# Kernel optimization log

Hardware: AMD Instinct MI355X
Metric: run time of the kernel (lower is better)

## Reference

```python
import jax, jax.numpy as jnp
import numpy as np

N = 1_000_000   # pose-graph nodes
E = 2_000_000   # edges (odometry + loop closures)
M = N - 1
L1, L2, L3, L4 = 1.0, 0.1, 1.0, 0.1  # loss weights
EPS = 1e-8

# ---- quaternion / Lie-group helpers (pypose convention: [x,y,z,w]) ----

def qmul(q, r):
    qv, qw = q[..., :3], q[..., 3:]
    rv, rw = r[..., :3], r[..., 3:]
    w = qw * rw - jnp.sum(qv * rv, axis=-1, keepdims=True)
    v = qw * rv + rw * qv + jnp.cross(qv, rv)
    return jnp.concatenate([v, w], axis=-1)

def qconj(q):  # inverse of a unit quaternion
    return jnp.concatenate([-q[..., :3], q[..., 3:]], axis=-1)

def qrot(q, v):  # rotate vector v by unit quaternion q
    qv, qw = q[..., :3], q[..., 3:]
    t = 2.0 * jnp.cross(qv, v)
    return v + qw * t + jnp.cross(qv, t)

def so3_log(q):  # SO3 -> so3 rotation vector phi
    v, w = q[..., :3], q[..., 3]
    n = jnp.linalg.norm(v, axis=-1)
    theta = 2.0 * jnp.arctan2(n, w)
    big = n > EPS
    k = jnp.where(big, theta / jnp.where(big, n, 1.0), 2.0 / jnp.where(jnp.abs(w) > EPS, w, 1.0))
    return v * k[..., None]

def se3_log(t, q):  # SE3 -> se3 = [tau(3), phi(3)] (translation first, pypose order)
    phi = so3_log(q)
    theta2 = jnp.sum(phi * phi, axis=-1)
    theta = jnp.sqrt(theta2)
    small = theta < 1e-4
    ts = jnp.where(small, 1.0, theta)
    # V^{-1} coefficient: 1/theta^2 - (1+cos)/(2 theta sin); Taylor -> 1/12
    coef = jnp.where(small, 1.0 / 12.0,
                     1.0 / jnp.where(small, 1.0, theta2)
                     - (1.0 + jnp.cos(ts)) / (2.0 * ts * jnp.sin(ts)))
    pxt = jnp.cross(phi, t)
    tau = t - 0.5 * pxt + coef[..., None] * jnp.cross(phi, pxt)  # V^{-1} t without 3x3 mats
    return jnp.concatenate([tau, phi], axis=-1)

def _unit_quat(key, n):
    q = jax.random.normal(key, (n, 4), dtype=jnp.float32)
    return q / jnp.linalg.norm(q, axis=-1, keepdims=True)

def setup_inputs() -> dict:
    key = jax.random.key(0)
    k = jax.random.split(key, 9)
    nodes = jnp.concatenate([jax.random.normal(k[0], (N, 3), jnp.float32), _unit_quat(k[1], N)], axis=-1)
    vels = jax.random.normal(k[2], (N, 3), jnp.float32)
    edges = jax.random.randint(k[3], (E, 2), 0, N, dtype=jnp.int32)
    poses = jnp.concatenate([jax.random.normal(k[4], (E, 3), jnp.float32), _unit_quat(k[5], E)], axis=-1)
    imu_drots = _unit_quat(k[6], M)
    imu_dtrans = 0.1 * jax.random.normal(k[7], (M, 3), jnp.float32)
    imu_dvels = 0.1 * jax.random.normal(k[8], (M, 3), jnp.float32)
    dts = jnp.full((M, 1), 0.05, dtype=jnp.float32)
    return dict(edges=edges, nodes=nodes, vels=vels, poses=poses,
                imu_drots=imu_drots, imu_dtrans=imu_dtrans, imu_dvels=imu_dvels, dts=dts)

def reference(edges, nodes, vels, poses, imu_drots, imu_dtrans, imu_dvels, dts):
    t_n, q_n = nodes[:, :3], nodes[:, 3:]
    # --- pose-graph residual: (poses^-1 o node1^-1 o node2).Log() ---
    n1 = nodes[edges[:, 0]]
    n2 = nodes[edges[:, 1]]
    t1, q1 = n1[:, :3], n1[:, 3:]
    t2, q2 = n2[:, :3], n2[:, 3:]
    tp, qp = poses[:, :3], poses[:, 3:]
    qi1 = qconj(q1)
    ti1 = -qrot(qi1, t1)           # node1^-1
    qa = qmul(qi1, q2)
    ta = ti1 + qrot(qi1, t2)       # node1^-1 o node2
    qip = qconj(qp)
    tip = -qrot(qip, tp)           # poses^-1
    qe = qmul(qip, qa)
    te = tip + qrot(qip, ta)
    pgerr = se3_log(te, qe)                                   # [E, 6]
    # --- adjacent velocity residual ---
    adjvelerr = imu_dvels - (vels[1:] - vels[:-1])            # [M, 3]
    # --- IMU rotation residual: (drot^-1 o R1^-1 o R2).Log() ---
    qre = qmul(qconj(imu_drots), qmul(qconj(q_n[:-1]), q_n[1:]))
    imuroterr = so3_log(qre)                                  # [M, 3]
    # --- translation/velocity residual ---
    transvelerr = (t_n[1:] - t_n[:-1]) - (vels[:-1] * dts + imu_dtrans)  # [M, 3]
    return jnp.concatenate([L1 * pgerr.ravel(), L2 * adjvelerr.ravel(),
                            L3 * imuroterr.ravel(), L4 * transvelerr.ravel()], axis=0)
```

## Files before the change

### kernel.cpp

```cpp
#include <hip/hip_runtime.h>
#include <math.h>

#define EPS_Q 1e-8f

struct F3 { float x, y, z; };
struct Q4 { F3 v; float w; };

typedef float fvec4 __attribute__((ext_vector_type(4)));

__device__ __forceinline__ F3 add3(F3 a, F3 b){ return {a.x+b.x, a.y+b.y, a.z+b.z}; }
__device__ __forceinline__ F3 sub3(F3 a, F3 b){ return {a.x-b.x, a.y-b.y, a.z-b.z}; }
__device__ __forceinline__ F3 scal3(float s, F3 a){ return {s*a.x, s*a.y, s*a.z}; }
__device__ __forceinline__ float dot3(F3 a, F3 b){ return a.x*b.x + a.y*b.y + a.z*b.z; }
__device__ __forceinline__ F3 cross3(F3 a, F3 b){
    return { a.y*b.z - a.z*b.y, a.z*b.x - a.x*b.z, a.x*b.y - a.y*b.x };
}

__device__ __forceinline__ Q4 qmul(Q4 q, Q4 r){
    Q4 o;
    o.w = q.w*r.w - dot3(q.v, r.v);
    o.v = add3(add3(scal3(q.w, r.v), scal3(r.w, q.v)), cross3(q.v, r.v));
    return o;
}
__device__ __forceinline__ Q4 qconj(Q4 q){ return { {-q.v.x, -q.v.y, -q.v.z}, q.w }; }
__device__ __forceinline__ F3 qrot(Q4 q, F3 v){
    F3 t = scal3(2.0f, cross3(q.v, v));
    return add3(add3(v, scal3(q.w, t)), cross3(q.v, t));
}
__device__ __forceinline__ F3 so3_log(Q4 q){
    float n = sqrtf(dot3(q.v, q.v));
    float theta = 2.0f * atan2f(n, q.w);
    float k;
    if (n > EPS_Q) k = theta / n;
    else           k = 2.0f / ((fabsf(q.w) > EPS_Q) ? q.w : 1.0f);
    return scal3(k, q.v);
}

__device__ __forceinline__ float ntl (const float* p){ return __builtin_nontemporal_load(p); }
__device__ __forceinline__ int   ntli(const int*   p){ return __builtin_nontemporal_load(p); }
__device__ __forceinline__ void  nts (float* p, float v){ __builtin_nontemporal_store(v, p); }

__global__ __launch_bounds__(256)
void fused_kernel(const int*   __restrict__ edges,
                  const float* __restrict__ nodes,
                  const float* __restrict__ vels,
                  const float* __restrict__ poses,
                  const float* __restrict__ imu_drots,
                  const float* __restrict__ imu_dtrans,
                  const float* __restrict__ imu_dvels,
                  const float* __restrict__ dts,
                  float*       __restrict__ out,
                  int E, int M, int NB, int T,
                  size_t off_adjvel, size_t off_imurot, size_t off_transvel)
{
    const int b   = blockIdx.x;
    const int tid = threadIdx.x;
    const long long f0 = ((long long)b       * NB) / T;
    const long long f1 = ((long long)(b + 1) * NB) / T;

    if (f1 > f0) {
        const int m = (int)f0 * 256 + tid;
        if (m >= M) return;

        const float* n0  = nodes + 7*(size_t)m;
        const float* n1p = nodes + 7*(size_t)(m+1);
        F3 t0 = {n0[0],  n0[1],  n0[2]};   Q4 q0 = {{n0[3],  n0[4],  n0[5]},  n0[6]};
        F3 t1 = {n1p[0], n1p[1], n1p[2]};  Q4 q1 = {{n1p[3], n1p[4], n1p[5]}, n1p[6]};

        F3 v0 = {vels[3*(size_t)m],     vels[3*(size_t)m + 1], vels[3*(size_t)m + 2]};
        F3 v1 = {vels[3*(size_t)m + 3], vels[3*(size_t)m + 4], vels[3*(size_t)m + 5]};

        fvec4 drq = __builtin_nontemporal_load(reinterpret_cast<const fvec4*>(imu_drots) + m);
        Q4 dr = {{drq.x, drq.y, drq.z}, drq.w};

        F3 dvm = { ntl(imu_dvels + 3*(size_t)m),
                   ntl(imu_dvels + 3*(size_t)m + 1),
                   ntl(imu_dvels + 3*(size_t)m + 2) };
        F3 dtr = { ntl(imu_dtrans + 3*(size_t)m),
                   ntl(imu_dtrans + 3*(size_t)m + 1),
                   ntl(imu_dtrans + 3*(size_t)m + 2) };
        float dt = ntl(dts + m);

        F3 adjv = sub3(dvm, sub3(v1, v0));
        nts(out + off_adjvel + 3*(size_t)m,     0.1f * adjv.x);
        nts(out + off_adjvel + 3*(size_t)m + 1, 0.1f * adjv.y);
        nts(out + off_adjvel + 3*(size_t)m + 2, 0.1f * adjv.z);

        Q4 qre = qmul(qconj(dr), qmul(qconj(q0), q1));
        F3 rot = so3_log(qre);
        nts(out + off_imurot + 3*(size_t)m,     rot.x);
        nts(out + off_imurot + 3*(size_t)m + 1, rot.y);
        nts(out + off_imurot + 3*(size_t)m + 2, rot.z);

        F3 tv = sub3(sub3(t1, t0), add3(scal3(dt, v0), dtr));
        nts(out + off_transvel + 3*(size_t)m,     0.1f * tv.x);
        nts(out + off_transvel + 3*(size_t)m + 1, 0.1f * tv.y);
        nts(out + off_transvel + 3*(size_t)m + 2, 0.1f * tv.z);
    } else {
        const int e = (b - (int)f0) * 256 + tid;
        if (e >= E) return;

        int i = ntli(edges + 2*(size_t)e);
        int j = ntli(edges + 2*(size_t)e + 1);
        const float* n1 = nodes + 7*(size_t)i;
        const float* n2 = nodes + 7*(size_t)j;
        const float* p  = poses + 7*(size_t)e;

        F3 t1 = {n1[0], n1[1], n1[2]};  Q4 q1 = {{n1[3], n1[4], n1[5]}, n1[6]};
        F3 t2 = {n2[0], n2[1], n2[2]};  Q4 q2 = {{n2[3], n2[4], n2[5]}, n2[6]};
        F3 tp = {ntl(p+0), ntl(p+1), ntl(p+2)};
        Q4 qp = {{ntl(p+3), ntl(p+4), ntl(p+5)}, ntl(p+6)};

        Q4 qi1 = qconj(q1);
        F3 ti1 = scal3(-1.0f, qrot(qi1, t1));
        Q4 qa  = qmul(qi1, q2);
        F3 ta  = add3(ti1, qrot(qi1, t2));

        Q4 qip = qconj(qp);
        F3 tip = scal3(-1.0f, qrot(qip, tp));
        Q4 qe  = qmul(qip, qa);
        F3 te  = add3(tip, qrot(qip, ta));

        F3 phi = so3_log(qe);
        float theta2 = dot3(phi, phi);
        float theta  = sqrtf(theta2);
        float coef;
        if (theta < 1e-4f) {
            coef = 1.0f / 12.0f;
        } else {
            float s, c;
            sincosf(theta, &s, &c);
            coef = 1.0f / theta2 - (1.0f + c) / (2.0f * theta * s);
        }
        F3 pxt = cross3(phi, te);
        F3 tau = add3(sub3(te, scal3(0.5f, pxt)), scal3(coef, cross3(phi, pxt)));

        float* o = out + 6*(size_t)e;
        nts(o,   tau.x); nts(o+1, tau.y); nts(o+2, tau.z);
        nts(o+3, phi.x); nts(o+4, phi.y); nts(o+5, phi.z);
    }
}

extern "C" void kernel_launch(void* const* d_in, const int* in_sizes, int n_in,
                              void* d_out, int out_size, void* d_ws, size_t ws_size,
                              hipStream_t stream) {
    const int*   edges      = (const int*)  d_in[0];
    const float* nodes      = (const float*)d_in[1];
    const float* vels       = (const float*)d_in[2];
    const float* poses      = (const float*)d_in[3];
    const float* imu_drots  = (const float*)d_in[4];
    const float* imu_dtrans = (const float*)d_in[5];
    const float* imu_dvels  = (const float*)d_in[6];
    const float* dts        = (const float*)d_in[7];
    float* out = (float*)d_out;

    const int E = in_sizes[0] / 2;
    const int M = in_sizes[7];

    const size_t off_adjvel   = 6*(size_t)E;
    const size_t off_imurot   = off_adjvel + 3*(size_t)M;
    const size_t off_transvel = off_imurot + 3*(size_t)M;

    const int BLK = 256;
    const int EB = (E + BLK - 1) / BLK;
    const int NB = (M + BLK - 1) / BLK;
    const int T  = EB + NB;

    fused_kernel<<<T, BLK, 0, stream>>>(edges, nodes, vels, poses,
                                        imu_drots, imu_dtrans, imu_dvels, dts,
                                        out, E, M, NB, T,
                                        off_adjvel, off_imurot, off_transvel);
}
```

Measured before the change: 275.9 us.

## Pack nodes into fp16 16-byte rows before the edge gather kernel

```diff
diff --git a/kernel.cpp b/kernel.cpp
--- a/kernel.cpp
+++ b/kernel.cpp
@@ -1,4 +1,5 @@
 #include <hip/hip_runtime.h>
+#include <hip/hip_fp16.h>
 #include <math.h>
 
 #define EPS_Q 1e-8f
@@ -6,7 +7,9 @@
 struct F3 { float x, y, z; };
 struct Q4 { F3 v; float w; };
 
-typedef float fvec4 __attribute__((ext_vector_type(4)));
+typedef float    fvec4 __attribute__((ext_vector_type(4)));
+typedef unsigned uvec4 __attribute__((ext_vector_type(4)));
+typedef int      ivec2 __attribute__((ext_vector_type(2)));
 
 __device__ __forceinline__ F3 add3(F3 a, F3 b){ return {a.x+b.x, a.y+b.y, a.z+b.z}; }
 __device__ __forceinline__ F3 sub3(F3 a, F3 b){ return {a.x-b.x, a.y-b.y, a.z-b.z}; }
@@ -37,108 +40,156 @@
 }
 
 __device__ __forceinline__ float ntl (const float* p){ return __builtin_nontemporal_load(p); }
-__device__ __forceinline__ int   ntli(const int*   p){ return __builtin_nontemporal_load(p); }
 __device__ __forceinline__ void  nts (float* p, float v){ __builtin_nontemporal_store(v, p); }
 
+__device__ __forceinline__ unsigned pack2h(float a, float b){
+    __half2 h = __floats2half2_rn(a, b);
+    unsigned u; __builtin_memcpy(&u, &h, 4);
+    return u;
+}
+__device__ __forceinline__ float2 unp2h(unsigned u){
+    __half2 h; __builtin_memcpy(&h, &u, 4);
+    return __half22float2(h);
+}
+
+template<bool PACK>
 __global__ __launch_bounds__(256)
-void fused_kernel(const int*   __restrict__ edges,
-                  const float* __restrict__ nodes,
-                  const float* __restrict__ vels,
-                  const float* __restrict__ poses,
-                  const float* __restrict__ imu_drots,
-                  const float* __restrict__ imu_dtrans,
-                  const float* __restrict__ imu_dvels,
-                  const float* __restrict__ dts,
-                  float*       __restrict__ out,
-                  int E, int M, int NB, int T,
-                  size_t off_adjvel, size_t off_imurot, size_t off_transvel)
-{
-    const int b   = blockIdx.x;
-    const int tid = threadIdx.x;
-    const long long f0 = ((long long)b       * NB) / T;
-    const long long f1 = ((long long)(b + 1) * NB) / T;
-
-    if (f1 > f0) {
-        const int m = (int)f0 * 256 + tid;
-        if (m >= M) return;
-
-        const float* n0  = nodes + 7*(size_t)m;
-        const float* n1p = nodes + 7*(size_t)(m+1);
-        F3 t0 = {n0[0],  n0[1],  n0[2]};   Q4 q0 = {{n0[3],  n0[4],  n0[5]},  n0[6]};
-        F3 t1 = {n1p[0], n1p[1], n1p[2]};  Q4 q1 = {{n1p[3], n1p[4], n1p[5]}, n1p[6]};
-
-        F3 v0 = {vels[3*(size_t)m],     vels[3*(size_t)m + 1], vels[3*(size_t)m + 2]};
-        F3 v1 = {vels[3*(size_t)m + 3], vels[3*(size_t)m + 4], vels[3*(size_t)m + 5]};
-
-        fvec4 drq = __builtin_nontemporal_load(reinterpret_cast<const fvec4*>(imu_drots) + m);
-        Q4 dr = {{drq.x, drq.y, drq.z}, drq.w};
-
-        F3 dvm = { ntl(imu_dvels + 3*(size_t)m),
-                   ntl(imu_dvels + 3*(size_t)m + 1),
-                   ntl(imu_dvels + 3*(size_t)m + 2) };
-        F3 dtr = { ntl(imu_dtrans + 3*(size_t)m),
-                   ntl(imu_dtrans + 3*(size_t)m + 1),
-                   ntl(imu_dtrans + 3*(size_t)m + 2) };
-        float dt = ntl(dts + m);
-
-        F3 adjv = sub3(dvm, sub3(v1, v0));
-        nts(out + off_adjvel + 3*(size_t)m,     0.1f * adjv.x);
-        nts(out + off_adjvel + 3*(size_t)m + 1, 0.1f * adjv.y);
-        nts(out + off_adjvel + 3*(size_t)m + 2, 0.1f * adjv.z);
-
-        Q4 qre = qmul(qconj(dr), qmul(qconj(q0), q1));
-        F3 rot = so3_log(qre);
-        nts(out + off_imurot + 3*(size_t)m,     rot.x);
-        nts(out + off_imurot + 3*(size_t)m + 1, rot.y);
-        nts(out + off_imurot + 3*(size_t)m + 2, rot.z);
-
-        F3 tv = sub3(sub3(t1, t0), add3(scal3(dt, v0), dtr));
-        nts(out + off_transvel + 3*(size_t)m,     0.1f * tv.x);
-        nts(out + off_transvel + 3*(size_t)m + 1, 0.1f * tv.y);
-        nts(out + off_transvel + 3*(size_t)m + 2, 0.1f * tv.z);
+void prep_kernel(const float* __restrict__ nodes,
+                 const float* __restrict__ vels,
+                 const float* __restrict__ imu_drots,
+                 const float* __restrict__ imu_dtrans,
+                 const float* __restrict__ imu_dvels,
+                 const float* __restrict__ dts,
+                 float*       __restrict__ out,
+                 uvec4*       __restrict__ nodes16,
+                 int N, int M,
+                 size_t off_adjvel, size_t off_imurot, size_t off_transvel)
+{
+    const int m = blockIdx.x * 256 + threadIdx.x;
+    if (m >= N) return;
+
+    const float* n0 = nodes + 7*(size_t)m;
+    F3 t0 = {n0[0], n0[1], n0[2]};  Q4 q0 = {{n0[3], n0[4], n0[5]}, n0[6]};
+
+    if (PACK) {
+        uvec4 row = { pack2h(t0.x, t0.y), pack2h(t0.z, 0.0f),
+                      pack2h(q0.v.x, q0.v.y), pack2h(q0.v.z, q0.w) };
+        nodes16[m] = row;
+    }
+
+    if (m >= M) return;
+
+    const float* n1p = nodes + 7*(size_t)(m+1);
+    F3 t1 = {n1p[0], n1p[1], n1p[2]};  Q4 q1 = {{n1p[3], n1p[4], n1p[5]}, n1p[6]};
+
+    F3 v0 = {vels[3*(size_t)m],     vels[3*(size_t)m + 1], vels[3*(size_t)m + 2]};
+    F3 v1 = {vels[3*(size_t)m + 3], vels[3*(size_t)m + 4], vels[3*(size_t)m + 5]};
+
+    fvec4 drq = __builtin_nontemporal_load(reinterpret_cast<const fvec4*>(imu_drots) + m);
+    Q4 dr = {{drq.x, drq.y, drq.z}, drq.w};
+
+    F3 dvm = { ntl(imu_dvels + 3*(size_t)m),
+               ntl(imu_dvels + 3*(size_t)m + 1),
+               ntl(imu_dvels + 3*(size_t)m + 2) };
+    F3 dtr = { ntl(imu_dtrans + 3*(size_t)m),
+               ntl(imu_dtrans + 3*(size_t)m + 1),
+               ntl(imu_dtrans + 3*(size_t)m + 2) };
+    float dt = ntl(dts + m);
+
+    F3 adjv = sub3(dvm, sub3(v1, v0));
+    nts(out + off_adjvel + 3*(size_t)m,     0.1f * adjv.x);
+    nts(out + off_adjvel + 3*(size_t)m + 1, 0.1f * adjv.y);
+    nts(out + off_adjvel + 3*(size_t)m + 2, 0.1f * adjv.z);
+
+    Q4 qre = qmul(qconj(dr), qmul(qconj(q0), q1));
+    F3 rot = so3_log(qre);
+    nts(out + off_imurot + 3*(size_t)m,     rot.x);
+    nts(out + off_imurot + 3*(size_t)m + 1, rot.y);
+    nts(out + off_imurot + 3*(size_t)m + 2, rot.z);
+
+    F3 tv = sub3(sub3(t1, t0), add3(scal3(dt, v0), dtr));
+    nts(out + off_transvel + 3*(size_t)m,     0.1f * tv.x);
+    nts(out + off_transvel + 3*(size_t)m + 1, 0.1f * tv.y);
+    nts(out + off_transvel + 3*(size_t)m + 2, 0.1f * tv.z);
+}
+
+__device__ __forceinline__ void edge_body(F3 t1, Q4 q1, F3 t2, Q4 q2,
+                                          const float* __restrict__ p,
+                                          float* __restrict__ o)
+{
+    F3 tp = {ntl(p+0), ntl(p+1), ntl(p+2)};
+    Q4 qp = {{ntl(p+3), ntl(p+4), ntl(p+5)}, ntl(p+6)};
+
+    Q4 qi1 = qconj(q1);
+    F3 ti1 = scal3(-1.0f, qrot(qi1, t1));
+    Q4 qa  = qmul(qi1, q2);
+    F3 ta  = add3(ti1, qrot(qi1, t2));
+
+    Q4 qip = qconj(qp);
+    F3 tip = scal3(-1.0f, qrot(qip, tp));
+    Q4 qe  = qmul(qip, qa);
+    F3 te  = add3(tip, qrot(qip, ta));
+
+    F3 phi = so3_log(qe);
+    float theta2 = dot3(phi, phi);
+    float theta  = sqrtf(theta2);
+    float coef;
+    if (theta < 1e-4f) {
+        coef = 1.0f / 12.0f;
     } else {
-        const int e = (b - (int)f0) * 256 + tid;
-        if (e >= E) return;
-
-        int i = ntli(edges + 2*(size_t)e);
-        int j = ntli(edges + 2*(size_t)e + 1);
-        const float* n1 = nodes + 7*(size_t)i;
-        const float* n2 = nodes + 7*(size_t)j;
-        const float* p  = poses + 7*(size_t)e;
-
-        F3 t1 = {n1[0], n1[1], n1[2]};  Q4 q1 = {{n1[3], n1[4], n1[5]}, n1[6]};
-        F3 t2 = {n2[0], n2[1], n2[2]};  Q4 q2 = {{n2[3], n2[4], n2[5]}, n2[6]};
-        F3 tp = {ntl(p+0), ntl(p+1), ntl(p+2)};
-        Q4 qp = {{ntl(p+3), ntl(p+4), ntl(p+5)}, ntl(p+6)};
-
-        Q4 qi1 = qconj(q1);
-        F3 ti1 = scal3(-1.0f, qrot(qi1, t1));
-        Q4 qa  = qmul(qi1, q2);
-        F3 ta  = add3(ti1, qrot(qi1, t2));
-
-        Q4 qip = qconj(qp);
-        F3 tip = scal3(-1.0f, qrot(qip, tp));
-        Q4 qe  = qmul(qip, qa);
-        F3 te  = add3(tip, qrot(qip, ta));
-
-        F3 phi = so3_log(qe);
-        float theta2 = dot3(phi, phi);
-        float theta  = sqrtf(theta2);
-        float coef;
-        if (theta < 1e-4f) {
-            coef = 1.0f / 12.0f;
-        } else {
-            float s, c;
-            sincosf(theta, &s, &c);
-            coef = 1.0f / theta2 - (1.0f + c) / (2.0f * theta * s);
-        }
-        F3 pxt = cross3(phi, te);
-        F3 tau = add3(sub3(te, scal3(0.5f, pxt)), scal3(coef, cross3(phi, pxt)));
-
-        float* o = out + 6*(size_t)e;
-        nts(o,   tau.x); nts(o+1, tau.y); nts(o+2, tau.z);
-        nts(o+3, phi.x); nts(o+4, phi.y); nts(o+5, phi.z);
+        float s, c;
+        sincosf(theta, &s, &c);
+        coef = 1.0f / theta2 - (1.0f + c) / (2.0f * theta * s);
     }
+    F3 pxt = cross3(phi, te);
+    F3 tau = add3(sub3(te, scal3(0.5f, pxt)), scal3(coef, cross3(phi, pxt)));
+
+    nts(o,   tau.x); nts(o+1, tau.y); nts(o+2, tau.z);
+    nts(o+3, phi.x); nts(o+4, phi.y); nts(o+5, phi.z);
+}
+
+__global__ __launch_bounds__(256)
+void edge_kernel_packed(const int*   __restrict__ edges,
+                        const uvec4* __restrict__ nodes16,
+                        const float* __restrict__ poses,
+                        float*       __restrict__ out,
+                        int E)
+{
+    const int e = blockIdx.x * 256 + threadIdx.x;
+    if (e >= E) return;
+
+    ivec2 ij = __builtin_nontemporal_load(reinterpret_cast<const ivec2*>(edges) + e);
+
+    uvec4 r1 = nodes16[ij.x];
+    uvec4 r2 = nodes16[ij.y];
+
+    float2 a0 = unp2h(r1.x), a1 = unp2h(r1.y), a2 = unp2h(r1.z), a3 = unp2h(r1.w);
+    float2 b0 = unp2h(r2.x), b1 = unp2h(r2.y), b2 = unp2h(r2.z), b3 = unp2h(r2.w);
+
+    F3 t1 = {a0.x, a0.y, a1.x};  Q4 q1 = {{a2.x, a2.y, a3.x}, a3.y};
+    F3 t2 = {b0.x, b0.y, b1.x};  Q4 q2 = {{b2.x, b2.y, b3.x}, b3.y};
+
+    edge_body(t1, q1, t2, q2, poses + 7*(size_t)e, out + 6*(size_t)e);
+}
+
+__global__ __launch_bounds__(256)
+void edge_kernel_direct(const int*   __restrict__ edges,
+                        const float* __restrict__ nodes,
+                        const float* __restrict__ poses,
+                        float*       __restrict__ out,
+                        int E)
+{
+    const int e = blockIdx.x * 256 + threadIdx.x;
+    if (e >= E) return;
+
+    ivec2 ij = __builtin_nontemporal_load(reinterpret_cast<const ivec2*>(edges) + e);
+    const float* n1 = nodes + 7*(size_t)ij.x;
+    const float* n2 = nodes + 7*(size_t)ij.y;
+
+    F3 t1 = {n1[0], n1[1], n1[2]};  Q4 q1 = {{n1[3], n1[4], n1[5]}, n1[6]};
+    F3 t2 = {n2[0], n2[1], n2[2]};  Q4 q2 = {{n2[3], n2[4], n2[5]}, n2[6]};
+
+    edge_body(t1, q1, t2, q2, poses + 7*(size_t)e, out + 6*(size_t)e);
 }
 
 extern "C" void kernel_launch(void* const* d_in, const int* in_sizes, int n_in,
@@ -155,6 +206,7 @@
     float* out = (float*)d_out;
 
     const int E = in_sizes[0] / 2;
+    const int N = in_sizes[1] / 7;
     const int M = in_sizes[7];
 
     const size_t off_adjvel   = 6*(size_t)E;
@@ -162,12 +214,21 @@
     const size_t off_transvel = off_imurot + 3*(size_t)M;
 
     const int BLK = 256;
-    const int EB = (E + BLK - 1) / BLK;
-    const int NB = (M + BLK - 1) / BLK;
-    const int T  = EB + NB;
-
-    fused_kernel<<<T, BLK, 0, stream>>>(edges, nodes, vels, poses,
-                                        imu_drots, imu_dtrans, imu_dvels, dts,
-                                        out, E, M, NB, T,
-                                        off_adjvel, off_imurot, off_transvel);
-}
+    const int NBLKS = (N + BLK - 1) / BLK;
+    const int EBLKS = (E + BLK - 1) / BLK;
+
+    uvec4* nodes16 = (uvec4*)d_ws;
+    const bool can_pack = (d_ws != nullptr) && (ws_size >= (size_t)N * 16);
+
+    if (can_pack) {
+        prep_kernel<true><<<NBLKS, BLK, 0, stream>>>(nodes, vels, imu_drots, imu_dtrans,
+                                                     imu_dvels, dts, out, nodes16, N, M,
+                                                     off_adjvel, off_imurot, off_transvel);
+        edge_kernel_packed<<<EBLKS, BLK, 0, stream>>>(edges, nodes16, poses, out, E);
+    } else {
+        prep_kernel<false><<<NBLKS, BLK, 0, stream>>>(nodes, vels, imu_drots, imu_dtrans,
+                                                      imu_dvels, dts, out, nullptr, N, M,
+                                                      off_adjvel, off_imurot, off_transvel);
+        edge_kernel_direct<<<EBLKS, BLK, 0, stream>>>(edges, nodes, poses, out, E);
+    }
+}
```

After: 263.9 us. 1.05x faster.
